# Optimization experiments

Hardware: AMD Instinct MI355X
Metric: run time of the kernel (lower is better)

The kernel has to match this reference:

```python
import jax, jax.numpy as jnp
import numpy as np
from jax import lax

B, CIN, H, W = 4096, 3, 64, 64
NVAR = 50

def _lin(x, w, b):
    return jax.nn.relu(x @ w + b)

def setup_inputs() -> dict:
    key = jax.random.key(0)
    ks = jax.random.split(key, 16)
    def rn(k, shape, scale=0.05):
        return jax.random.normal(k, shape, dtype=jnp.float32) * scale
    return {
        "x": jax.random.normal(ks[0], (B, CIN, H, W), dtype=jnp.float32),
        "C": jax.random.uniform(ks[1], (B, NVAR, NVAR), dtype=jnp.float32),
        "conv1_w": rn(ks[2], (32, CIN, 3, 3)), "conv1_b": jnp.zeros((32,), jnp.float32),
        "conv2_w": rn(ks[3], (64, 32, 3, 3)), "conv2_b": jnp.zeros((64,), jnp.float32),
        "enc_w": rn(ks[4], (64, 128)), "enc_b": jnp.zeros((128,), jnp.float32),
        "f1_w": rn(ks[5], (128, NVAR)), "f1_b": jnp.zeros((NVAR,), jnp.float32),
        "f2_w": rn(ks[6], (NVAR, 128)), "f2_b": jnp.zeros((128,), jnp.float32),
        "f3_w": rn(ks[7], (256, 64)), "f3_b": jnp.zeros((64,), jnp.float32),
        "f4_w": rn(ks[8], (64, 64)), "f4_b": jnp.zeros((64,), jnp.float32),
        "f5_w": rn(ks[9], (64, 64)), "f5_b": jnp.zeros((64,), jnp.float32),
        "out_w": rn(ks[10], (64, NVAR)), "out_b": jnp.zeros((NVAR,), jnp.float32),
    }

def reference(x, C, conv1_w, conv1_b, conv2_w, conv2_b, enc_w, enc_b,
              f1_w, f1_b, f2_w, f2_b, f3_w, f3_b, f4_w, f4_b, f5_w, f5_b,
              out_w, out_b):
    dn = ("NCHW", "OIHW", "NCHW")
    # Observation_Encoder_F: conv(s2)->relu->conv(s2)->relu->global mean pool->linear->relu
    h = lax.conv_general_dilated(x, conv1_w, (2, 2), ((1, 1), (1, 1)), dimension_numbers=dn)
    h = jax.nn.relu(h + conv1_b[None, :, None, None])          # [B,32,32,32]
    h = lax.conv_general_dilated(h, conv2_w, (2, 2), ((1, 1), (1, 1)), dimension_numbers=dn)
    h = jax.nn.relu(h + conv2_b[None, :, None, None])          # [B,64,16,16]
    x1 = _lin(h.mean(axis=(2, 3)), enc_w, enc_b)               # [B,128]
    x2 = _lin(x1, f1_w, f1_b)                                  # [B,V]
    # per-sample causal matrix multiply: e[b] = C[b] @ x2[b]
    e = jnp.einsum("bij,bj->bi", C, x2)                        # [B,V]
    x3 = _lin(e, f2_w, f2_b)                                   # [B,128]
    x4 = jnp.concatenate((x1, x3), axis=1)                     # [B,256]
    x5 = _lin(x4, f3_w, f3_b)
    x6 = _lin(x5, f4_w, f4_b)
    x7 = _lin(x6, f5_w, f5_b)
    return jax.nn.softmax(_lin(x7, out_w, out_b), axis=1)      # [B,V]
```

## Files before the change

### kernel.cpp

```cpp
#include <hip/hip_runtime.h>
#include <hip/hip_bf16.h>


typedef __attribute__((ext_vector_type(8)))  short short8;
typedef __attribute__((ext_vector_type(16))) float floatx16;

#define AS1 __attribute__((address_space(1)))
#define AS3 __attribute__((address_space(3)))

#define BAR_LGKM() asm volatile("s_waitcnt lgkmcnt(0)\ns_barrier" ::: "memory")
#define BAR_FULL() asm volatile("s_waitcnt vmcnt(0) lgkmcnt(0)\ns_barrier" ::: "memory")

__device__ __forceinline__ short f2bf(float f) {
    unsigned u = __float_as_uint(f);
    u += 0x7fffu + ((u >> 16) & 1u);
    return (short)(u >> 16);
}

__device__ __forceinline__ float rl(float v, int i) {
    return __int_as_float(__builtin_amdgcn_readlane(__float_as_int(v), i));
}

__device__ __forceinline__ unsigned pkbf2(float a, float b) {
    float2 fp; fp.x = a; fp.y = b;
    __hip_bfloat162 bb = __float22bfloat162_rn(fp);
    return *(unsigned*)&bb;
}

__global__ void k_prep(const float* __restrict__ cw2, const float* __restrict__ cw1,
                       short* __restrict__ packw) {
    const int idx = blockIdx.x * 256 + threadIdx.x;
    if (idx < 9 * 64 * 32) {
        const int ic  = idx & 31;
        const int oc  = (idx >> 5) & 63;
        const int pos = idx >> 11;
        packw[idx] = f2bf(cw2[oc * 288 + ic * 9 + pos]);
    } else if (idx < 9 * 64 * 32 + 32 * 32) {
        const int j  = idx - 9 * 64 * 32;
        const int k  = j & 31;
        const int oc = j >> 5;
        packw[idx] = (k < 27) ? f2bf(cw1[oc * 27 + k]) : (short)0;
    }
}

#define XS_OFF  0
#define A1_OFF  49152
#define A1STR   80
#define H1_OFF  90112
#define ROWB    2064
#define SMEM_SZ (49152 + 40960 + 66048)
#define SPB     16

__global__ __launch_bounds__(512, 2) void k_conv(
    const float* __restrict__ x,    const float* __restrict__ c1b,
    const short* __restrict__ packw, const float* __restrict__ c2b,
    float* __restrict__ pooled)
{
    __shared__ __align__(16) char smem[SMEM_SZ];
    float* xs      = (float*)(smem + XS_OFF);
    char*  a1      = smem + A1_OFF;
    char*  h1b     = smem + H1_OFF;
    float* poolbuf = (float*)(smem + A1_OFF);

    const int tid  = threadIdx.x;
    const int lane = tid & 63;
    const int w    = tid >> 6;

    const int col = lane & 31;
    const int ss  = lane >> 5;

    const int nt  = w & 1;
    const int ox2 = lane & 15;
    const int oyb = (lane >> 4) & 1;
    const int ocn = nt * 32 + col;
    const float bias2 = c2b[ocn];

    short8 z8;
    #pragma unroll
    for (int i = 0; i < 8; ++i) z8[i] = 0;

    short8 bfr[9][2];
    #pragma unroll
    for (int pos = 0; pos < 9; ++pos)
        #pragma unroll
        for (int h = 0; h < 2; ++h)
            bfr[pos][h] = *(const short8*)(packw + (pos * 64 + ocn) * 32 + h * 16 + ss * 8);

    const short* w1p = packw + 18432;
    short8 w1f[2];
    #pragma unroll
    for (int k = 0; k < 2; ++k)
        w1f[k] = *(const short8*)(w1p + col * 32 + k * 16 + ss * 8);

    float2 b1p[8];
    #pragma unroll
    for (int rp = 0; rp < 8; ++rp)
        b1p[rp] = *(const float2*)(c1b + ((rp & 1) * 2 + (rp >> 1) * 8 + 4 * ss));

    int  sbv[3][2];
    bool okx[3];
    #pragma unroll
    for (int kx = 0; kx < 3; ++kx) {
        const int ph   = (kx + 1) & 1;
        const int xh   = ox2 - (kx == 0 ? 1 : 0);
        const int slot = ph * 16 + xh;
        const int swz  = (slot >> 1) & 3;
        okx[kx] = (xh >= 0);
        #pragma unroll
        for (int h = 0; h < 2; ++h)
            sbv[kx][h] = slot * 64 + (((ss + 2 * h) ^ swz) << 4);
    }

    const int slotpx = ((col & 1) << 4) + (col >> 1);
    const int wswz   = (slotpx >> 1) & 3;
    const int wbase  = slotpx * 64 + ss * 8;

    auto prefetch_x = [&](int bb) {
        const char* g = (const char*)(x + (size_t)bb * 12288);
        #pragma unroll
        for (int i = 0; i < 6; ++i) {
            const int off = (w * 6 + i) << 10;
            __builtin_amdgcn_global_load_lds(
                (const AS1 unsigned int*)(g + off + lane * 16),
                (AS3 unsigned int*)(smem + XS_OFF + off), 16, 0, 0);
        }
    };

    auto im2col = [&](int half) {
        const int p  = tid;
        const int oy = half * 16 + (p >> 5);
        const int ox = p & 31;
        float f[32];
        #pragma unroll
        for (int ic = 0; ic < 3; ++ic) {
            #pragma unroll
            for (int ky = 0; ky < 3; ++ky) {
                const int  iy   = 2 * oy + ky - 1;
                const bool oky  = iy >= 0;
                const int  base = ic * 4096 + (oky ? iy : 0) * 64 + 2 * ox;
                const float2 p12 = *(const float2*)(xs + base);
                const float2 pm  = *(const float2*)(xs + (base >= 2 ? base - 2 : 0));
                const int k = ic * 9 + ky * 3;
                f[k + 0] = (oky && ox > 0) ? pm.y : 0.f;
                f[k + 1] = oky ? p12.x : 0.f;
                f[k + 2] = oky ? p12.y : 0.f;
            }
        }
        f[27] = 0.f; f[28] = 0.f; f[29] = 0.f; f[30] = 0.f; f[31] = 0.f;
        unsigned pk[16];
        #pragma unroll
        for (int t = 0; t < 16; ++t) pk[t] = pkbf2(f[2 * t], f[2 * t + 1]);
        uint4* dst = (uint4*)(a1 + p * A1STR);
        dst[0] = make_uint4(pk[0],  pk[1],  pk[2],  pk[3]);
        dst[1] = make_uint4(pk[4],  pk[5],  pk[6],  pk[7]);
        dst[2] = make_uint4(pk[8],  pk[9],  pk[10], pk[11]);
        dst[3] = make_uint4(pk[12], pk[13], pk[14], pk[15]);
    };

    auto conv1_mfma = [&](int half) {
        #pragma unroll
        for (int i = 0; i < 2; ++i) {
            const int t = w * 2 + i;
            const char* abase = a1 + (t * 32 + col) * A1STR + ss * 16;
            const short8 bf0 = *(const short8*)(abase);
            const short8 bf1 = *(const short8*)(abase + 32);
            floatx16 acc;
            #pragma unroll
            for (int r = 0; r < 16; ++r) acc[r] = 0.f;
            acc = __builtin_amdgcn_mfma_f32_32x32x16_bf16(w1f[0], bf0, acc, 0, 0, 0);
            acc = __builtin_amdgcn_mfma_f32_32x32x16_bf16(w1f[1], bf1, acc, 0, 0, 0);
            const int oyg = half * 16 + t;
            char* hb = h1b + oyg * ROWB + wbase;
            #pragma unroll
            for (int rp = 0; rp < 8; ++rp) {
                const unsigned u = pkbf2(fmaxf(acc[2 * rp]     + b1p[rp].x, 0.f),
                                         fmaxf(acc[2 * rp + 1] + b1p[rp].y, 0.f));
                const int off = (((rp >> 1) ^ wswz) << 4) + (rp & 1) * 4;
                *(unsigned*)(hb + off) = u;
            }
        }
    };

    prefetch_x(blockIdx.x);

    #pragma unroll 1
    for (int s = 0; s < SPB; ++s) {
        const int b = blockIdx.x + (s << 8);

        BAR_FULL();
        im2col(0);
        BAR_LGKM();
        conv1_mfma(0);
        BAR_LGKM();
        im2col(1);
        BAR_LGKM();
        if (s + 1 < SPB) prefetch_x(blockIdx.x + ((s + 1) << 8));
        conv1_mfma(1);
        BAR_LGKM();

        const int t0 = w >> 1;
        float pool = 0.f;
        floatx16 acc0, acc1;
        #pragma unroll
        for (int r = 0; r < 16; ++r) { acc0[r] = 0.f; acc1[r] = 0.f; }
        #pragma unroll
        for (int ky = 0; ky < 3; ++ky) {
            #pragma unroll
            for (int kx = 0; kx < 3; ++kx) {
                const int  iy0 = t0 * 4 + oyb * 2 + ky - 1;
                const bool ok0 = okx[kx] && (iy0 >= 0);
                const bool ok1 = okx[kx];
                const int  ba0 = iy0 * ROWB;
                const int  ba1 = ba0 + 16 * ROWB;
                #pragma unroll
                for (int h = 0; h < 2; ++h) {
                    const int so = sbv[kx][h];
                    short8 a0v = ok0 ? *(const short8*)(h1b + ba0 + so) : z8;
                    short8 a1v = ok1 ? *(const short8*)(h1b + ba1 + so) : z8;
                    const short8 bf = bfr[ky * 3 + kx][h];
                    acc0 = __builtin_amdgcn_mfma_f32_32x32x16_bf16(a0v, bf, acc0, 0, 0, 0);
                    acc1 = __builtin_amdgcn_mfma_f32_32x32x16_bf16(a1v, bf, acc1, 0, 0, 0);
                }
            }
        }
        #pragma unroll
        for (int r = 0; r < 16; ++r) {
            pool += fmaxf(acc0[r] + bias2, 0.f);
            pool += fmaxf(acc1[r] + bias2, 0.f);
        }
        pool += __shfl_xor(pool, 32, 64);
        if (lane < 32) poolbuf[w * 32 + lane] = pool;
        BAR_LGKM();
        if (tid < 64) {
            const int g = tid >> 5, c = tid & 31;
            pooled[(size_t)b * 64 + tid] =
                (poolbuf[(g    ) * 32 + c] + poolbuf[(g + 2) * 32 + c] +
                 poolbuf[(g + 4) * 32 + c] + poolbuf[(g + 6) * 32 + c]) * (1.f / 256.f);
        }
    }
}

__global__ __launch_bounds__(256, 4) void k_mlp(
    const float* __restrict__ pooled, const float* __restrict__ C,
    const float* __restrict__ ew, const float* __restrict__ eb,
    const float* __restrict__ w1, const float* __restrict__ b1,
    const float* __restrict__ w2, const float* __restrict__ b2,
    const float* __restrict__ w3, const float* __restrict__ b3,
    const float* __restrict__ w4, const float* __restrict__ b4,
    const float* __restrict__ w5, const float* __restrict__ b5,
    const float* __restrict__ ow, const float* __restrict__ ob,
    float* __restrict__ out)
{
    const int lane = threadIdx.x & 63;
    const int w    = threadIdx.x >> 6;
    const int b    = blockIdx.x * 4 + w;
    const int jc   = (lane < 50) ? lane : 0;

    const float p0 = pooled[(size_t)b * 64 + lane];

    float x1a = eb[lane], x1b = eb[lane + 64];
    #pragma unroll 8
    for (int i = 0; i < 64; ++i) {
        const float ai = rl(p0, i);
        x1a += ai * ew[i * 128 + lane];
        x1b += ai * ew[i * 128 + 64 + lane];
    }
    x1a = fmaxf(x1a, 0.f); x1b = fmaxf(x1b, 0.f);

    float x2 = b1[jc];
    #pragma unroll 8
    for (int i = 0; i < 64; ++i)  x2 += rl(x1a, i) * w1[i * 50 + jc];
    #pragma unroll 8
    for (int i = 0; i < 64; ++i)  x2 += rl(x1b, i) * w1[(64 + i) * 50 + jc];
    x2 = fmaxf(x2, 0.f);

    const float2* C2 = (const float2*)(C + (size_t)b * 2500 + jc * 50);
    float e = 0.f;
    #pragma unroll 5
    for (int j = 0; j < 25; ++j) {
        const float2 cc = C2[j];
        e += cc.x * rl(x2, 2 * j) + cc.y * rl(x2, 2 * j + 1);
    }

    float x3a = b2[lane], x3b = b2[lane + 64];
    #pragma unroll 10
    for (int i = 0; i < 50; ++i) {
        const float ai = rl(e, i);
        x3a += ai * w2[i * 128 + lane];
        x3b += ai * w2[i * 128 + 64 + lane];
    }
    x3a = fmaxf(x3a, 0.f); x3b = fmaxf(x3b, 0.f);

    float x5 = b3[lane];
    #pragma unroll 8
    for (int i = 0; i < 64; ++i) x5 += rl(x1a, i) * w3[(i      ) * 64 + lane];
    #pragma unroll 8
    for (int i = 0; i < 64; ++i) x5 += rl(x1b, i) * w3[(64  + i) * 64 + lane];
    #pragma unroll 8
    for (int i = 0; i < 64; ++i) x5 += rl(x3a, i) * w3[(128 + i) * 64 + lane];
    #pragma unroll 8
    for (int i = 0; i < 64; ++i) x5 += rl(x3b, i) * w3[(192 + i) * 64 + lane];
    x5 = fmaxf(x5, 0.f);

    float x6 = b4[lane];
    #pragma unroll 8
    for (int i = 0; i < 64; ++i) x6 += rl(x5, i) * w4[i * 64 + lane];
    x6 = fmaxf(x6, 0.f);
    float x7 = b5[lane];
    #pragma unroll 8
    for (int i = 0; i < 64; ++i) x7 += rl(x6, i) * w5[i * 64 + lane];
    x7 = fmaxf(x7, 0.f);

    float lg = ob[jc];
    #pragma unroll 8
    for (int i = 0; i < 64; ++i) lg += rl(x7, i) * ow[i * 50 + jc];
    float z = (lane < 50) ? fmaxf(lg, 0.f) : -1e30f;

    float m = z;
    #pragma unroll
    for (int o = 32; o > 0; o >>= 1) m = fmaxf(m, __shfl_xor(m, o, 64));
    float pr = __expf(z - m);
    float sden = pr;
    #pragma unroll
    for (int o = 32; o > 0; o >>= 1) sden += __shfl_xor(sden, o, 64);

    if (lane < 50) out[(size_t)b * 50 + lane] = pr / sden;
}

extern "C" void kernel_launch(void* const* d_in, const int* in_sizes, int n_in,
                              void* d_out, int out_size, void* d_ws, size_t ws_size,
                              hipStream_t stream) {
    (void)in_sizes; (void)n_in; (void)out_size; (void)ws_size;
    const float* x   = (const float*)d_in[0];
    const float* Cm  = (const float*)d_in[1];
    const float* c1w = (const float*)d_in[2];
    const float* c1b = (const float*)d_in[3];
    const float* c2w = (const float*)d_in[4];
    const float* c2b = (const float*)d_in[5];
    const float* ew  = (const float*)d_in[6];
    const float* ebv = (const float*)d_in[7];
    const float* f1w = (const float*)d_in[8];
    const float* f1b = (const float*)d_in[9];
    const float* f2w = (const float*)d_in[10];
    const float* f2b = (const float*)d_in[11];
    const float* f3w = (const float*)d_in[12];
    const float* f3b = (const float*)d_in[13];
    const float* f4w = (const float*)d_in[14];
    const float* f4b = (const float*)d_in[15];
    const float* f5w = (const float*)d_in[16];
    const float* f5b = (const float*)d_in[17];
    const float* ow  = (const float*)d_in[18];
    const float* ob  = (const float*)d_in[19];

    short* packw  = (short*)d_ws;
    float* pooled = (float*)((char*)d_ws + 65536);
    float* out    = (float*)d_out;

    hipLaunchKernelGGL(k_prep, dim3(76),   dim3(256), 0, stream, c2w, c1w, packw);
    hipLaunchKernelGGL(k_conv, dim3(256),  dim3(512), 0, stream, x, c1b, packw, c2b, pooled);
    hipLaunchKernelGGL(k_mlp,  dim3(1024), dim3(256), 0, stream, pooled, Cm,
                       ew, ebv, f1w, f1b, f2w, f2b, f3w, f3b, f4w, f4b, f5w, f5b,
                       ow, ob, out);
}
```

Before: 396.6 us.

## Rewrite MLP head as bf16 MFMA over 16-sample tiles with LDS-staged weights

The prep kernel now also packs all MLP weights into padded, transposed bf16 blocks plus a concatenated bias array in workspace. The MLP kernel processes 16 samples per block: it bulk-loads the packed weights into LDS with global_load_lds, then computes each dense layer with 16x16x32 bf16 MFMA. Activations stay in LDS between layers, and the softmax runs per 16-lane group. This replaces the scalar readlane FMA chain, which re-read the fp32 weights from global memory for every sample. In exchange it uses bf16 weights and activations, which costs accuracy, and each block copies about 140KB of weights into LDS with only one block per CU.

```diff
diff --git a/kernel.cpp b/kernel.cpp
--- a/kernel.cpp
+++ b/kernel.cpp
@@ -3,6 +3,7 @@
 
 
 typedef __attribute__((ext_vector_type(8)))  short short8;
+typedef __attribute__((ext_vector_type(4)))  float floatx4;
 typedef __attribute__((ext_vector_type(16))) float floatx16;
 
 #define AS1 __attribute__((address_space(1)))
@@ -17,29 +18,65 @@
     return (short)(u >> 16);
 }
 
-__device__ __forceinline__ float rl(float v, int i) {
-    return __int_as_float(__builtin_amdgcn_readlane(__float_as_int(v), i));
-}
-
 __device__ __forceinline__ unsigned pkbf2(float a, float b) {
     float2 fp; fp.x = a; fp.y = b;
     __hip_bfloat162 bb = __float22bfloat162_rn(fp);
     return *(unsigned*)&bb;
 }
 
+#define WS_MLP_B    40960
+#define WS_BIAS_B   (40960 + 115712)
+#define WS_POOL_B   163840
+
 __global__ void k_prep(const float* __restrict__ cw2, const float* __restrict__ cw1,
-                       short* __restrict__ packw) {
+                       const float* __restrict__ ew,  const float* __restrict__ w1,
+                       const float* __restrict__ w2,  const float* __restrict__ w3,
+                       const float* __restrict__ w4,  const float* __restrict__ w5,
+                       const float* __restrict__ ow,  const float* __restrict__ eb,
+                       const float* __restrict__ b1,  const float* __restrict__ b2,
+                       const float* __restrict__ b3,  const float* __restrict__ b4,
+                       const float* __restrict__ b5,  const float* __restrict__ ob,
+                       short* __restrict__ packw, float* __restrict__ biasout) {
     const int idx = blockIdx.x * 256 + threadIdx.x;
-    if (idx < 9 * 64 * 32) {
+    if (idx < 18432) {
         const int ic  = idx & 31;
         const int oc  = (idx >> 5) & 63;
         const int pos = idx >> 11;
         packw[idx] = f2bf(cw2[oc * 288 + ic * 9 + pos]);
-    } else if (idx < 9 * 64 * 32 + 32 * 32) {
-        const int j  = idx - 9 * 64 * 32;
+    } else if (idx < 19456) {
+        const int j  = idx - 18432;
         const int k  = j & 31;
         const int oc = j >> 5;
         packw[idx] = (k < 27) ? f2bf(cw1[oc * 27 + k]) : (short)0;
+    } else if (idx < 77312) {
+        const int e = idx - 19456;
+        short v;
+        if (e < 9216)        { const int n = e / 72,  kk = e - n * 72;
+            v = (kk < 64) ? f2bf(ew[kk * 128 + n]) : (short)0; }
+        else if (e < 17920)  { const int r = e - 9216;  const int n = r / 136, kk = r - n * 136;
+            v = (kk < 128 && n < 50) ? f2bf(w1[kk * 50 + n]) : (short)0; }
+        else if (e < 27136)  { const int r = e - 17920; const int n = r / 72,  kk = r - n * 72;
+            v = (kk < 50) ? f2bf(w2[kk * 128 + n]) : (short)0; }
+        else if (e < 44032)  { const int r = e - 27136; const int n = r / 264, kk = r - n * 264;
+            v = (kk < 256) ? f2bf(w3[kk * 64 + n]) : (short)0; }
+        else if (e < 48640)  { const int r = e - 44032; const int n = r / 72,  kk = r - n * 72;
+            v = (kk < 64) ? f2bf(w4[kk * 64 + n]) : (short)0; }
+        else if (e < 53248)  { const int r = e - 48640; const int n = r / 72,  kk = r - n * 72;
+            v = (kk < 64) ? f2bf(w5[kk * 64 + n]) : (short)0; }
+        else                 { const int r = e - 53248; const int n = r / 72,  kk = r - n * 72;
+            v = (kk < 64 && n < 50) ? f2bf(ow[kk * 50 + n]) : (short)0; }
+        packw[20480 + e] = v;
+    } else if (idx < 77888) {
+        const int j = idx - 77312;
+        float v;
+        if (j < 128)      v = eb[j];
+        else if (j < 192) v = (j - 128 < 50) ? b1[j - 128] : 0.f;
+        else if (j < 320) v = b2[j - 192];
+        else if (j < 384) v = b3[j - 320];
+        else if (j < 448) v = b4[j - 384];
+        else if (j < 512) v = b5[j - 448];
+        else              v = (j - 512 < 50) ? ob[j - 512] : 0.f;
+        biasout[j] = v;
     }
 }
 
@@ -240,91 +277,132 @@
     }
 }
 
-__global__ __launch_bounds__(256, 4) void k_mlp(
+#define ML_BIAS_B 115712
+#define ML_P_SH   59392
+#define ML_A_SH   60544
+#define ML_B_SH   64768
+#define ML_Z_F    34496
+#define ML_SMEM   142336
+
+__global__ __launch_bounds__(256, 1) void k_mlp(
+    const char* __restrict__ wsblk,
     const float* __restrict__ pooled, const float* __restrict__ C,
-    const float* __restrict__ ew, const float* __restrict__ eb,
-    const float* __restrict__ w1, const float* __restrict__ b1,
-    const float* __restrict__ w2, const float* __restrict__ b2,
-    const float* __restrict__ w3, const float* __restrict__ b3,
-    const float* __restrict__ w4, const float* __restrict__ b4,
-    const float* __restrict__ w5, const float* __restrict__ b5,
-    const float* __restrict__ ow, const float* __restrict__ ob,
     float* __restrict__ out)
 {
-    const int lane = threadIdx.x & 63;
-    const int w    = threadIdx.x >> 6;
-    const int b    = blockIdx.x * 4 + w;
-    const int jc   = (lane < 50) ? lane : 0;
-
-    const float p0 = pooled[(size_t)b * 64 + lane];
-
-    float x1a = eb[lane], x1b = eb[lane + 64];
-    #pragma unroll 8
-    for (int i = 0; i < 64; ++i) {
-        const float ai = rl(p0, i);
-        x1a += ai * ew[i * 128 + lane];
-        x1b += ai * ew[i * 128 + 64 + lane];
-    }
-    x1a = fmaxf(x1a, 0.f); x1b = fmaxf(x1b, 0.f);
-
-    float x2 = b1[jc];
-    #pragma unroll 8
-    for (int i = 0; i < 64; ++i)  x2 += rl(x1a, i) * w1[i * 50 + jc];
-    #pragma unroll 8
-    for (int i = 0; i < 64; ++i)  x2 += rl(x1b, i) * w1[(64 + i) * 50 + jc];
-    x2 = fmaxf(x2, 0.f);
-
-    const float2* C2 = (const float2*)(C + (size_t)b * 2500 + jc * 50);
-    float e = 0.f;
-    #pragma unroll 5
-    for (int j = 0; j < 25; ++j) {
-        const float2 cc = C2[j];
-        e += cc.x * rl(x2, 2 * j) + cc.y * rl(x2, 2 * j + 1);
-    }
-
-    float x3a = b2[lane], x3b = b2[lane + 64];
-    #pragma unroll 10
-    for (int i = 0; i < 50; ++i) {
-        const float ai = rl(e, i);
-        x3a += ai * w2[i * 128 + lane];
-        x3b += ai * w2[i * 128 + 64 + lane];
-    }
-    x3a = fmaxf(x3a, 0.f); x3b = fmaxf(x3b, 0.f);
-
-    float x5 = b3[lane];
-    #pragma unroll 8
-    for (int i = 0; i < 64; ++i) x5 += rl(x1a, i) * w3[(i      ) * 64 + lane];
-    #pragma unroll 8
-    for (int i = 0; i < 64; ++i) x5 += rl(x1b, i) * w3[(64  + i) * 64 + lane];
-    #pragma unroll 8
-    for (int i = 0; i < 64; ++i) x5 += rl(x3a, i) * w3[(128 + i) * 64 + lane];
-    #pragma unroll 8
-    for (int i = 0; i < 64; ++i) x5 += rl(x3b, i) * w3[(192 + i) * 64 + lane];
-    x5 = fmaxf(x5, 0.f);
-
-    float x6 = b4[lane];
-    #pragma unroll 8
-    for (int i = 0; i < 64; ++i) x6 += rl(x5, i) * w4[i * 64 + lane];
-    x6 = fmaxf(x6, 0.f);
-    float x7 = b5[lane];
-    #pragma unroll 8
-    for (int i = 0; i < 64; ++i) x7 += rl(x6, i) * w5[i * 64 + lane];
-    x7 = fmaxf(x7, 0.f);
-
-    float lg = ob[jc];
-    #pragma unroll 8
-    for (int i = 0; i < 64; ++i) lg += rl(x7, i) * ow[i * 50 + jc];
-    float z = (lane < 50) ? fmaxf(lg, 0.f) : -1e30f;
-
-    float m = z;
-    #pragma unroll
-    for (int o = 32; o > 0; o >>= 1) m = fmaxf(m, __shfl_xor(m, o, 64));
-    float pr = __expf(z - m);
-    float sden = pr;
-    #pragma unroll
-    for (int o = 32; o > 0; o >>= 1) sden += __shfl_xor(sden, o, 64);
-
-    if (lane < 50) out[(size_t)b * 50 + lane] = pr / sden;
+    __shared__ __align__(16) char smem[ML_SMEM];
+    short*       Sw   = (short*)smem;
+    const short* S    = (const short*)smem;
+    const float* Bias = (const float*)(smem + ML_BIAS_B);
+    float*       Zf   = (float*)smem;
+
+    const int tid    = threadIdx.x;
+    const int lane   = tid & 63;
+    const int w      = tid >> 6;
+    const int n16    = lane & 15;
+    const int q      = lane >> 4;
+    const int tile16 = blockIdx.x * 16;
+
+    #pragma unroll
+    for (int i = 0; i < 29; ++i) {
+        const int off = i * 4096 + w * 1024;
+        __builtin_amdgcn_global_load_lds(
+            (const AS1 unsigned int*)(wsblk + off + lane * 16),
+            (AS3 unsigned int*)(smem + off), 16, 0, 0);
+    }
+    {
+        const float4 pv = *(const float4*)(pooled + tile16 * 64 + tid * 4);
+        const int s = tid >> 4, k = (tid & 15) * 4;
+        uint2 u;
+        u.x = pkbf2(pv.x, pv.y);
+        u.y = pkbf2(pv.z, pv.w);
+        *(uint2*)(Sw + ML_P_SH + s * 72 + k) = u;
+    }
+    BAR_FULL();
+
+    auto layer = [&](int inOff, int inPitch, int K, int wOff, int nTiles,
+                     int biasOff, int outOff, bool isOut) {
+        #pragma unroll
+        for (int nt = w; nt < nTiles; nt += 4) {
+            floatx4 acc;
+            acc[0] = 0.f; acc[1] = 0.f; acc[2] = 0.f; acc[3] = 0.f;
+            const int kp = K + 8;
+            #pragma unroll
+            for (int kc = 0; kc < 8; ++kc) {
+                if (kc * 32 >= K) break;
+                const short8 aF = *(const short8*)(S + inOff + n16 * inPitch + kc * 32 + q * 8);
+                const short8 bF = *(const short8*)(S + wOff + (nt * 16 + n16) * kp + kc * 32 + q * 8);
+                acc = __builtin_amdgcn_mfma_f32_16x16x32_bf16(aF, bF, acc, 0, 0, 0);
+            }
+            const int   n  = nt * 16 + n16;
+            const float bv = Bias[biasOff + n];
+            #pragma unroll
+            for (int r = 0; r < 4; ++r) {
+                const int   m = q * 4 + r;
+                const float v = fmaxf(acc[r] + bv, 0.f);
+                if (isOut) Zf[ML_Z_F + m * 68 + n] = (n < 50) ? v : -1e30f;
+                else       Sw[outOff + m * 264 + n] = f2bf(v);
+            }
+        }
+    };
+
+    layer(ML_P_SH, 72, 64, 0, 8, 0, ML_A_SH, false);
+    BAR_LGKM();
+    layer(ML_A_SH, 264, 128, 9216, 4, 128, ML_B_SH, false);
+    BAR_LGKM();
+
+    #pragma unroll
+    for (int r = 0; r < 4; ++r) {
+        const int item = tid + r * 256;
+        if (item < 800) {
+            const int s = (item * 1311) >> 16;
+            const int i = item - s * 50;
+            const float* Cp = C + (size_t)(tile16 + s) * 2500 + i * 50;
+            float e = 0.f;
+            #pragma unroll
+            for (int j2 = 0; j2 < 25; ++j2) {
+                const float2   cc = *(const float2*)(Cp + 2 * j2);
+                const unsigned u  = *(const unsigned*)(S + ML_B_SH + s * 264 + 2 * j2);
+                e += cc.x * __uint_as_float(u << 16)
+                   + cc.y * __uint_as_float(u & 0xffff0000u);
+            }
+            Sw[ML_B_SH + s * 264 + 64 + i] = f2bf(e);
+        }
+    }
+    if ((tid & 15) < 14)
+        Sw[ML_B_SH + (tid >> 4) * 264 + 64 + 50 + (tid & 15)] = 0;
+    BAR_LGKM();
+
+    layer(ML_B_SH + 64, 264, 64, 17920, 8, 192, ML_A_SH + 128, false);
+    BAR_LGKM();
+    layer(ML_A_SH, 264, 256, 27136, 4, 320, ML_B_SH, false);
+    BAR_LGKM();
+    layer(ML_B_SH, 264, 64, 44032, 4, 384, ML_B_SH + 64, false);
+    BAR_LGKM();
+    layer(ML_B_SH + 64, 264, 64, 48640, 4, 448, ML_B_SH + 128, false);
+    BAR_LGKM();
+    layer(ML_B_SH + 128, 264, 64, 53248, 4, 512, 0, true);
+    BAR_LGKM();
+
+    {
+        const int s = tid >> 4, g = tid & 15;
+        const float4 zv = *(const float4*)(Zf + ML_Z_F + s * 68 + g * 4);
+        float m = fmaxf(fmaxf(zv.x, zv.y), fmaxf(zv.z, zv.w));
+        #pragma unroll
+        for (int o = 8; o > 0; o >>= 1) m = fmaxf(m, __shfl_xor(m, o, 16));
+        float4 p;
+        p.x = __expf(zv.x - m); p.y = __expf(zv.y - m);
+        p.z = __expf(zv.z - m); p.w = __expf(zv.w - m);
+        float sum = p.x + p.y + p.z + p.w;
+        #pragma unroll
+        for (int o = 8; o > 0; o >>= 1) sum += __shfl_xor(sum, o, 16);
+        const float inv = 1.f / sum;
+        float* po = out + (size_t)(tile16 + s) * 50 + g * 4;
+        const int j = g * 4;
+        if (j     < 50) po[0] = p.x * inv;
+        if (j + 1 < 50) po[1] = p.y * inv;
+        if (j + 2 < 50) po[2] = p.z * inv;
+        if (j + 3 < 50) po[3] = p.w * inv;
+    }
 }
 
 extern "C" void kernel_launch(void* const* d_in, const int* in_sizes, int n_in,
@@ -352,13 +430,17 @@
     const float* ow  = (const float*)d_in[18];
     const float* ob  = (const float*)d_in[19];
 
-    short* packw  = (short*)d_ws;
-    float* pooled = (float*)((char*)d_ws + 65536);
-    float* out    = (float*)d_out;
-
-    hipLaunchKernelGGL(k_prep, dim3(76),   dim3(256), 0, stream, c2w, c1w, packw);
-    hipLaunchKernelGGL(k_conv, dim3(256),  dim3(512), 0, stream, x, c1b, packw, c2b, pooled);
-    hipLaunchKernelGGL(k_mlp,  dim3(1024), dim3(256), 0, stream, pooled, Cm,
-                       ew, ebv, f1w, f1b, f2w, f2b, f3w, f3b, f4w, f4b, f5w, f5b,
-                       ow, ob, out);
-}
+    short* packw   = (short*)d_ws;
+    float* biasout = (float*)((char*)d_ws + WS_BIAS_B);
+    float* pooled  = (float*)((char*)d_ws + WS_POOL_B);
+    const char* wsblk = (const char*)d_ws + WS_MLP_B;
+    float* out     = (float*)d_out;
+
+    hipLaunchKernelGGL(k_prep, dim3(305), dim3(256), 0, stream,
+                       c2w, c1w, ew, f1w, f2w, f3w, f4w, f5w, ow,
+                       ebv, f1b, f2b, f3b, f4b, f5b, ob, packw, biasout);
+    hipLaunchKernelGGL(k_conv, dim3(256), dim3(512), 0, stream,
+                       x, c1b, packw, c2b, pooled);
+    hipLaunchKernelGGL(k_mlp,  dim3(256), dim3(256), 0, stream,
+                       wsblk, pooled, Cm, out);
+}
```

Result: faster. 361.5 us (-8.9%).
